# Performance work log

Measured on AMD Instinct MI355X. Metric: run time of the kernel, lower is better.

The kernel has to match this reference:

```python
import jax, jax.numpy as jnp
import numpy as np

N = 100000      # nodes
E = 3_200_000   # edges
F_IN = 256      # input feature dim
R = 16          # rank_bound (GCN output dim)
D = 128         # embedding_dim (trans output)
B = 16384       # batch of node indices
EPS = 1e-5


def setup_inputs() -> dict:
    key = jax.random.key(0)
    ks = jax.random.split(key, 9)
    x = jax.random.normal(ks[0], (N, F_IN), jnp.float32)
    edge_index = jax.random.randint(ks[1], (2, E), 0, N, dtype=jnp.int64)
    trans = jax.random.normal(ks[2], (R, D), jnp.float32) * 0.1
    batch = jax.random.randint(ks[3], (B,), 0, N, dtype=jnp.int64)
    W = jax.random.normal(ks[4], (R, F_IN), jnp.float32) / np.sqrt(F_IN).astype(np.float32)
    b = jnp.zeros((R,), jnp.float32)
    ln_w = jnp.ones((R,), jnp.float32)
    ln_b = jnp.zeros((R,), jnp.float32)
    prelu_a = jnp.full((1,), 0.25, jnp.float32)  # PReLU single shared slope
    return dict(x=x, edge_index=edge_index, trans=trans, batch=batch,
                W=W, b=b, ln_w=ln_w, ln_b=ln_b, prelu_a=prelu_a)


def gcn_conv(x, edge_index, W, b):
    # PyG GCNConv: lin first, then symmetric-normalized aggregation with self-loops.
    h = x @ W.T  # [N, R]
    loop = jnp.arange(N, dtype=edge_index.dtype)
    src = jnp.concatenate([edge_index[0], loop])  # messages flow src -> dst
    dst = jnp.concatenate([edge_index[1], loop])
    deg = jax.ops.segment_sum(jnp.ones_like(dst, h.dtype), dst, num_segments=N)
    dinv = jnp.where(deg > 0, jax.lax.rsqrt(deg), 0.0)
    norm = dinv[src] * dinv[dst]                   # [E+N]
    msg = h[src] * norm[:, None]                   # gather [E+N, R]
    out = jax.ops.segment_sum(msg, dst, num_segments=N)  # scatter-add
    return out + b


def reference(x, edge_index, trans, batch, W, b, ln_w, ln_b, prelu_a):
    h = gcn_conv(x, edge_index, W, b)              # [N, R]
    # PyG LayerNorm (graph mode): normalize over all nodes and channels.
    h = h - h.mean()
    var = (h * h).mean()
    h = h * jax.lax.rsqrt(var + EPS) * ln_w + ln_b
    # PReLU
    h = jnp.where(h >= 0, h, prelu_a * h)
    emb = h @ trans                                # [N, D]
    return emb[batch]                              # index_select(0, batch)
```

## Files before the change

### kernel.cpp

```cpp
#include <hip/hip_runtime.h>

#define EPS 1e-5f
#define BSHIFT 8
#define BSIZE  256
#define NBMAX  512
#define PCHUNK 8192
#define BCAP   16384
#define LCAP   12288

typedef short bf16x8 __attribute__((ext_vector_type(8)));
typedef float f32x4  __attribute__((ext_vector_type(4)));

__device__ __forceinline__ unsigned short f2bf(float f) {
    unsigned u = __float_as_uint(f);
    u += 0x7FFFu + ((u >> 16) & 1u);
    return (unsigned short)(u >> 16);
}
__device__ __forceinline__ float bf2f(unsigned short s) {
    return __uint_as_float(((unsigned)s) << 16);
}
__device__ __forceinline__ void acc8(float* acc, uint4 v) {
    acc[0] += bf2f((unsigned short)(v.x & 0xFFFFu)); acc[1] += bf2f((unsigned short)(v.x >> 16));
    acc[2] += bf2f((unsigned short)(v.y & 0xFFFFu)); acc[3] += bf2f((unsigned short)(v.y >> 16));
    acc[4] += bf2f((unsigned short)(v.z & 0xFFFFu)); acc[5] += bf2f((unsigned short)(v.z >> 16));
    acc[6] += bf2f((unsigned short)(v.w & 0xFFFFu)); acc[7] += bf2f((unsigned short)(v.w >> 16));
}
__device__ __forceinline__ void cvt_hilo(const float* f, bf16x8& hi, bf16x8& lo) {
#pragma unroll
    for (int j = 0; j < 8; j++) {
        unsigned short h = f2bf(f[j]);
        hi[j] = (short)h;
        lo[j] = (short)f2bf(f[j] - bf2f(h));
    }
}

__global__ __launch_bounds__(512) void k_init(unsigned* cursor, int NB) {
    int t = threadIdx.x;
    if (t < NB) cursor[t] = (unsigned)t * BCAP;
}

__global__ __launch_bounds__(512) void k_bpart(const int* __restrict__ ei,
                                               unsigned* __restrict__ cursor,
                                               unsigned* __restrict__ sorted, int E, int NB) {
    __shared__ unsigned cnt[NBMAX];
    __shared__ unsigned lbase[NBMAX];
    __shared__ unsigned loff[NBMAX + 1];
    __shared__ unsigned sh[512];
    __shared__ unsigned stage[PCHUNK];
    __shared__ unsigned short bkt[PCHUNK];
    int t = threadIdx.x;
    for (int i = t; i < NB; i += 512) cnt[i] = 0u;
    __syncthreads();
    const int4* src4 = (const int4*)ei;
    const int4* dst4 = (const int4*)(ei + E);
    int E4 = E >> 2;
    int base4 = blockIdx.x * (PCHUNK / 4);
#pragma unroll
    for (int i = 0; i < PCHUNK / 4 / 512; i++) {
        int idx = base4 + i * 512 + t;
        if (idx < E4) {
            int4 d = dst4[idx];
            atomicAdd(&cnt[d.x >> BSHIFT], 1u);
            atomicAdd(&cnt[d.y >> BSHIFT], 1u);
            atomicAdd(&cnt[d.z >> BSHIFT], 1u);
            atomicAdd(&cnt[d.w >> BSHIFT], 1u);
        }
    }
    __syncthreads();
    unsigned v = (t < NB) ? cnt[t] : 0u;
    sh[t] = v;
    if (t < NB) lbase[t] = v ? atomicAdd(&cursor[t], v) : 0u;
    __syncthreads();
    for (int off = 1; off < 512; off <<= 1) {
        unsigned a = (t >= off) ? sh[t - off] : 0u;
        __syncthreads();
        sh[t] += a;
        __syncthreads();
    }
    if (t < NB) { loff[t] = sh[t] - v; cnt[t] = 0u; }
    if (t == NB - 1) loff[NB] = sh[t];
    __syncthreads();
    for (int b = t; b < NB; b += 512) {
        unsigned s = loff[b], e2 = loff[b + 1];
        for (unsigned j = s; j < e2; j++) bkt[j] = (unsigned short)b;
    }
#pragma unroll
    for (int i = 0; i < PCHUNK / 4 / 512; i++) {
        int idx = base4 + i * 512 + t;
        if (idx < E4) {
            int4 s = src4[idx];
            int4 d = dst4[idx];
            int b; unsigned r;
            b = d.x >> BSHIFT; r = atomicAdd(&cnt[b], 1u);
            stage[loff[b] + r] = (unsigned)s.x | ((unsigned)(d.x & (BSIZE - 1)) << 17);
            b = d.y >> BSHIFT; r = atomicAdd(&cnt[b], 1u);
            stage[loff[b] + r] = (unsigned)s.y | ((unsigned)(d.y & (BSIZE - 1)) << 17);
            b = d.z >> BSHIFT; r = atomicAdd(&cnt[b], 1u);
            stage[loff[b] + r] = (unsigned)s.z | ((unsigned)(d.z & (BSIZE - 1)) << 17);
            b = d.w >> BSHIFT; r = atomicAdd(&cnt[b], 1u);
            stage[loff[b] + r] = (unsigned)s.w | ((unsigned)(d.w & (BSIZE - 1)) << 17);
        }
    }
    __syncthreads();
    unsigned total = loff[NB];
    for (unsigned i = t; i < total; i += 512) {
        unsigned b = bkt[i];
        sorted[lbase[b] + (i - loff[b])] = stage[i];
    }
}

__global__ __launch_bounds__(512) void k_bdeg2(const unsigned* __restrict__ cursor,
                                               const unsigned* __restrict__ sorted,
                                               unsigned* __restrict__ nstart,
                                               float* __restrict__ dinv, int N) {
    __shared__ unsigned deg[BSIZE];
    __shared__ unsigned wsum[4];
    int b = blockIdx.x, t = threadIdx.x;
    if (t < BSIZE) deg[t] = 0u;
    __syncthreads();
    unsigned s0 = (unsigned)b * BCAP, s1 = cursor[b];
    for (unsigned j = s0 + t; j < s1; j += 512)
        atomicAdd(&deg[sorted[j] >> 17], 1u);
    __syncthreads();
    unsigned d0 = 0, inc = 0;
    int lane = t & 63, wid = t >> 6;
    if (t < BSIZE) {
        d0 = deg[t];
        inc = d0;
        for (int off = 1; off < 64; off <<= 1) {
            unsigned u = __shfl_up(inc, off, 64);
            if (lane >= off) inc += u;
        }
        if (lane == 63) wsum[wid] = inc;
    }
    __syncthreads();
    if (t < BSIZE) {
        unsigned wbase = 0;
        for (int w = 0; w < wid; w++) wbase += wsum[w];
        unsigned excl = wbase + inc - d0;
        int node = (b << BSHIFT) + t;
        if (node < N) {
            nstart[node] = s0 + excl;
            dinv[node] = rsqrtf((float)(d0 + 1u));
        }
    }
}

__global__ __launch_bounds__(256, 4) void k_gemm(const float* __restrict__ x,
                                                 const float* __restrict__ W,
                                                 const float* __restrict__ dinv,
                                                 unsigned short* __restrict__ hs,
                                                 int N, int NT) {
    int t = threadIdx.x;
    int w = t >> 6, lane = t & 63;
    int lr = lane & 15;
    int lk = lane >> 4;
    bf16x8 bh[8], bl[8];
#pragma unroll
    for (int kt = 0; kt < 8; kt++) {
        float wf[8];
        const float* wp = W + lr * 256 + kt * 32 + lk * 8;
        *(float4*)&wf[0] = *(const float4*)wp;
        *(float4*)&wf[4] = *(const float4*)(wp + 4);
        cvt_hilo(wf, bh[kt], bl[kt]);
    }
    int nw = gridDim.x * 4;
    int wid = blockIdx.x * 4 + w;
    for (int tile = wid; tile < NT; tile += nw) {
        int nb = tile << 4;
        int node = nb + lr;
        const float* xp = x + (size_t)node * 256;
        f32x4 acc = {0.f, 0.f, 0.f, 0.f};
#pragma unroll
        for (int kt = 0; kt < 8; kt++) {
            float af[8];
            if (node < N) {
                const float* ap = xp + kt * 32 + lk * 8;
                *(float4*)&af[0] = *(const float4*)ap;
                *(float4*)&af[4] = *(const float4*)(ap + 4);
            } else {
#pragma unroll
                for (int j = 0; j < 8; j++) af[j] = 0.f;
            }
            bf16x8 ah, al;
            cvt_hilo(af, ah, al);
            acc = __builtin_amdgcn_mfma_f32_16x16x32_bf16(ah, bh[kt], acc, 0, 0, 0);
            acc = __builtin_amdgcn_mfma_f32_16x16x32_bf16(al, bh[kt], acc, 0, 0, 0);
            acc = __builtin_amdgcn_mfma_f32_16x16x32_bf16(ah, bl[kt], acc, 0, 0, 0);
        }
#pragma unroll
        for (int i = 0; i < 4; i++) {
            int n2 = nb + lk * 4 + i;
            if (n2 < N) {
                float dv = dinv[n2];
                hs[(size_t)n2 * 16 + lr] = f2bf(acc[i] * dv);
            }
        }
    }
}

__global__ __launch_bounds__(512) void k_aggf(const unsigned* __restrict__ cursor,
                                              const unsigned* __restrict__ nstart,
                                              const unsigned* __restrict__ sorted,
                                              const unsigned short* __restrict__ hs,
                                              const float* __restrict__ dinv,
                                              const float* __restrict__ bias,
                                              float* __restrict__ agg,
                                              float2* __restrict__ part,
                                              unsigned* __restrict__ scratch, int N) {
    __shared__ unsigned buf[LCAP];
    __shared__ unsigned cur0[BSIZE + 1];
    __shared__ unsigned curv[BSIZE];
    __shared__ float ss[8], qq[8];
    int b = blockIdx.x, t = threadIdx.x;
    unsigned s0 = (unsigned)b * BCAP, s1 = cursor[b];
    unsigned len = s1 - s0;
    if (t < BSIZE) {
        int node = (b << BSHIFT) + t;
        unsigned ns = (node < N) ? nstart[node] : s1;
        cur0[t] = ns - s0;
        curv[t] = ns - s0;
    }
    if (t == 0) cur0[BSIZE] = len;
    __syncthreads();
    bool fit = (len <= (unsigned)LCAP);
    if (fit) {
        for (unsigned j = t; j < len; j += 512) {
            unsigned u = sorted[s0 + j];
            unsigned pos = atomicAdd(&curv[u >> 17], 1u);
            buf[pos] = u & 0x1FFFFu;
        }
    } else {
        for (unsigned j = t; j < len; j += 512) {
            unsigned u = sorted[s0 + j];
            unsigned pos = atomicAdd(&curv[u >> 17], 1u);
            scratch[s0 + pos] = u & 0x1FFFFu;
        }
    }
    __syncthreads();
    int g = t >> 4, r = t & 15;
    int sub = r >> 1;
    int half = r & 1;
    float sacc = 0.f, qacc = 0.f;
#pragma unroll 1
    for (int p = 0; p < 8; p++) {
        int dloc = p * 32 + g;
        int d = (b << BSHIFT) + dloc;
        float acc[8];
#pragma unroll
        for (int c = 0; c < 8; c++) acc[c] = 0.f;
        if (d < N) {
            unsigned l0 = cur0[dloc], l1 = cur0[dloc + 1];
            for (unsigned j = l0; j < l1; j += 16) {
                unsigned row0 = j + sub, row1 = j + 8 + sub;
                bool p0 = row0 < l1, p1 = row1 < l1;
                unsigned i0 = 0, i1 = 0;
                if (fit) {
                    if (p0) i0 = buf[row0];
                    if (p1) i1 = buf[row1];
                } else {
                    if (p0) i0 = scratch[s0 + row0];
                    if (p1) i1 = scratch[s0 + row1];
                }
                uint4 v0, v1;
                if (p0) v0 = ((const uint4*)(hs + (size_t)i0 * 16))[half];
                if (p1) v1 = ((const uint4*)(hs + (size_t)i1 * 16))[half];
                if (p0) acc8(acc, v0);
                if (p1) acc8(acc, v1);
            }
        }
#pragma unroll
        for (int off = 2; off <= 8; off <<= 1) {
#pragma unroll
            for (int c = 0; c < 8; c++) acc[c] += __shfl_down(acc[c], off, 64);
        }
        if (d < N && r < 2) {
            float dd = dinv[d];
            uint4 hv = ((const uint4*)(hs + (size_t)d * 16))[half];
            float self[8];
            self[0] = bf2f((unsigned short)(hv.x & 0xFFFFu)); self[1] = bf2f((unsigned short)(hv.x >> 16));
            self[2] = bf2f((unsigned short)(hv.y & 0xFFFFu)); self[3] = bf2f((unsigned short)(hv.y >> 16));
            self[4] = bf2f((unsigned short)(hv.z & 0xFFFFu)); self[5] = bf2f((unsigned short)(hv.z >> 16));
            self[6] = bf2f((unsigned short)(hv.w & 0xFFFFu)); self[7] = bf2f((unsigned short)(hv.w >> 16));
            float o[8];
#pragma unroll
            for (int c = 0; c < 8; c++) o[c] = (acc[c] + self[c]) * dd;
            float* an = agg + (size_t)d * 16 + half * 8;
            *(float4*)(an)     = make_float4(o[0], o[1], o[2], o[3]);
            *(float4*)(an + 4) = make_float4(o[4], o[5], o[6], o[7]);
            const float* bp = bias + half * 8;
            float4 b0 = *(const float4*)bp, b1 = *(const float4*)(bp + 4);
            float a0 = o[0] + b0.x, a1 = o[1] + b0.y, a2 = o[2] + b0.z, a3 = o[3] + b0.w;
            float a4 = o[4] + b1.x, a5 = o[5] + b1.y, a6 = o[6] + b1.z, a7 = o[7] + b1.w;
            sacc += (a0 + a1) + (a2 + a3) + (a4 + a5) + (a6 + a7);
            qacc += a0 * a0 + a1 * a1 + a2 * a2 + a3 * a3 + a4 * a4 + a5 * a5 + a6 * a6 + a7 * a7;
        }
    }
    for (int off = 32; off > 0; off >>= 1) {
        sacc += __shfl_down(sacc, off, 64);
        qacc += __shfl_down(qacc, off, 64);
    }
    int lane = t & 63, wid = t >> 6;
    if (lane == 0) { ss[wid] = sacc; qq[wid] = qacc; }
    __syncthreads();
    if (t == 0) {
        float s = 0.f, q = 0.f;
#pragma unroll
        for (int i = 0; i < 8; i++) { s += ss[i]; q += qq[i]; }
        part[b] = make_float2(s, q);
    }
}

__global__ __launch_bounds__(256) void k_final(const float* __restrict__ agg,
                                               const int* __restrict__ batch,
                                               const float* __restrict__ trans,
                                               const float* __restrict__ bias,
                                               const float* __restrict__ ln_w,
                                               const float* __restrict__ ln_b,
                                               const float* __restrict__ prelu_a,
                                               const float2* __restrict__ part,
                                               float* __restrict__ out, int B, float invCnt, int M) {
    __shared__ float tl[16 * 128];
    __shared__ float hh[8 * 16];
    __shared__ float ssr[4], qqr[4];
    const int tid = threadIdx.x;
    for (int i = tid; i < 2048; i += 256) tl[i] = trans[i];
    float s = 0.f, q = 0.f;
    for (int i = tid; i < M; i += 256) {
        float2 v = part[i];
        s += v.x; q += v.y;
    }
    for (int off = 32; off > 0; off >>= 1) {
        s += __shfl_down(s, off, 64);
        q += __shfl_down(q, off, 64);
    }
    int lane = tid & 63, wd = tid >> 6;
    if (lane == 0) { ssr[wd] = s; qqr[wd] = q; }
    __syncthreads();
    float S = ssr[0] + ssr[1] + ssr[2] + ssr[3];
    float Q = qqr[0] + qqr[1] + qqr[2] + qqr[3];
    float mean = S * invCnt;
    float var  = Q * invCnt - mean * mean;
    float inv  = rsqrtf(var + EPS);
    int row0 = blockIdx.x * 8;
    if (tid < 128) {
        int lr = tid >> 4, r = tid & 15;
        int row = row0 + lr;
        if (row < B) {
            int node = batch[row];
            float v = agg[(size_t)node * 16 + r] + bias[r];
            v = (v - mean) * inv * ln_w[r] + ln_b[r];
            float a = prelu_a[0];
            v = v >= 0.f ? v : a * v;
            hh[lr * 16 + r] = v;
        }
    }
    __syncthreads();
    int d = tid & 127, hlf = tid >> 7;
    float tv[16];
#pragma unroll
    for (int r = 0; r < 16; r++) tv[r] = tl[r * 128 + d];
#pragma unroll
    for (int rr = 0; rr < 4; rr++) {
        int lr = rr * 2 + hlf;
        int row = row0 + lr;
        if (row < B) {
            const float* hrow = hh + lr * 16;
            float acc = 0.f;
#pragma unroll
            for (int r = 0; r < 16; r++) acc += hrow[r] * tv[r];
            out[(size_t)row * 128 + d] = acc;
        }
    }
}

extern "C" void kernel_launch(void* const* d_in, const int* in_sizes, int n_in,
                              void* d_out, int out_size, void* d_ws, size_t ws_size,
                              hipStream_t stream) {
    const float* x       = (const float*)d_in[0];
    const int*   ei      = (const int*)d_in[1];
    const float* trans   = (const float*)d_in[2];
    const int*   batch   = (const int*)d_in[3];
    const float* W       = (const float*)d_in[4];
    const float* bias    = (const float*)d_in[5];
    const float* ln_w    = (const float*)d_in[6];
    const float* ln_b    = (const float*)d_in[7];
    const float* prelu_a = (const float*)d_in[8];
    float* out = (float*)d_out;

    const int N = in_sizes[0] / 256;
    const int E = in_sizes[1] / 2;
    const int B = in_sizes[3];
    const int NB = (N + BSIZE - 1) >> BSHIFT;
    const int pbp = (E + PCHUNK - 1) / PCHUNK;
    const int NT = (N + 15) / 16;

    char* p = (char*)d_ws;
    unsigned short* hs = (unsigned short*)p;  p += (size_t)N * 16 * 2;
    float*    agg     = (float*)p;     p += (size_t)N * 16 * 4;
    unsigned* sorted  = (unsigned*)p;  p += (size_t)NB * BCAP * 4;
    unsigned* scratch = (unsigned*)p;  p += (size_t)NB * BCAP * 4;
    float*    dinv    = (float*)p;     p += (size_t)N * 4;
    unsigned* nstart  = (unsigned*)p;  p += (size_t)(N + 1) * 4;
    unsigned* cursor  = (unsigned*)p;  p += NBMAX * 4;
    p = (char*)(((size_t)p + 7) & ~(size_t)7);
    float2*   part    = (float2*)p;    p += (size_t)NB * 8;

    hipLaunchKernelGGL(k_init,  dim3(1),           dim3(512), 0, stream, cursor, NB);
    hipLaunchKernelGGL(k_bpart, dim3(pbp),         dim3(512), 0, stream, ei, cursor, sorted, E, NB);
    hipLaunchKernelGGL(k_bdeg2, dim3(NB),          dim3(512), 0, stream, cursor, sorted, nstart, dinv, N);
    hipLaunchKernelGGL(k_gemm,  dim3(512),         dim3(256), 0, stream, x, W, dinv, hs, N, NT);
    hipLaunchKernelGGL(k_aggf,  dim3(NB),          dim3(512), 0, stream, cursor, nstart, sorted, hs, dinv, bias, agg, part, scratch, N);
    hipLaunchKernelGGL(k_final, dim3((B + 7) / 8), dim3(256), 0, stream, agg, batch, trans, bias,
                       ln_w, ln_b, prelu_a, part, out, B, 1.0f / (float)(N * 16), NB);
}
```

Before: 264.0 us.

## Fold degree computation into partition pass and drop separate degree kernel

Eliminates the k_bdeg2 kernel, which reread the sorted edge buckets to count per-node degrees. Degrees are now counted with global atomics inside the partition kernel. The per-node prefix offsets and inverse sqrt degree are recomputed inside the aggregation kernel, and the GEMM computes rsqrt directly from the degree array. This saves one kernel launch and one pass over the bucketed edges, at the cost of 3.2M global atomic increments on a 100K-entry array and a larger k_init launch to zero it.

Measured after the change: 372.7 us. +41.2%, slower.

```diff
diff --git a/kernel.cpp b/kernel.cpp
--- a/kernel.cpp
+++ b/kernel.cpp
@@ -34,13 +34,16 @@
     }
 }
 
-__global__ __launch_bounds__(512) void k_init(unsigned* cursor, int NB) {
-    int t = threadIdx.x;
-    if (t < NB) cursor[t] = (unsigned)t * BCAP;
+__global__ __launch_bounds__(512) void k_init(unsigned* __restrict__ deg,
+                                              unsigned* __restrict__ cursor, int N, int NB) {
+    int idx = blockIdx.x * 512 + threadIdx.x;
+    if (idx < N) deg[idx] = 0u;
+    if (blockIdx.x == 0 && threadIdx.x < NB) cursor[threadIdx.x] = (unsigned)threadIdx.x * BCAP;
 }
 
 __global__ __launch_bounds__(512) void k_bpart(const int* __restrict__ ei,
                                                unsigned* __restrict__ cursor,
+                                               unsigned* __restrict__ deg,
                                                unsigned* __restrict__ sorted, int E, int NB) {
     __shared__ unsigned cnt[NBMAX];
     __shared__ unsigned lbase[NBMAX];
@@ -64,6 +67,10 @@
             atomicAdd(&cnt[d.y >> BSHIFT], 1u);
             atomicAdd(&cnt[d.z >> BSHIFT], 1u);
             atomicAdd(&cnt[d.w >> BSHIFT], 1u);
+            atomicAdd(&deg[d.x], 1u);
+            atomicAdd(&deg[d.y], 1u);
+            atomicAdd(&deg[d.z], 1u);
+            atomicAdd(&deg[d.w], 1u);
         }
     }
     __syncthreads();
@@ -109,46 +116,9 @@
     }
 }
 
-__global__ __launch_bounds__(512) void k_bdeg2(const unsigned* __restrict__ cursor,
-                                               const unsigned* __restrict__ sorted,
-                                               unsigned* __restrict__ nstart,
-                                               float* __restrict__ dinv, int N) {
-    __shared__ unsigned deg[BSIZE];
-    __shared__ unsigned wsum[4];
-    int b = blockIdx.x, t = threadIdx.x;
-    if (t < BSIZE) deg[t] = 0u;
-    __syncthreads();
-    unsigned s0 = (unsigned)b * BCAP, s1 = cursor[b];
-    for (unsigned j = s0 + t; j < s1; j += 512)
-        atomicAdd(&deg[sorted[j] >> 17], 1u);
-    __syncthreads();
-    unsigned d0 = 0, inc = 0;
-    int lane = t & 63, wid = t >> 6;
-    if (t < BSIZE) {
-        d0 = deg[t];
-        inc = d0;
-        for (int off = 1; off < 64; off <<= 1) {
-            unsigned u = __shfl_up(inc, off, 64);
-            if (lane >= off) inc += u;
-        }
-        if (lane == 63) wsum[wid] = inc;
-    }
-    __syncthreads();
-    if (t < BSIZE) {
-        unsigned wbase = 0;
-        for (int w = 0; w < wid; w++) wbase += wsum[w];
-        unsigned excl = wbase + inc - d0;
-        int node = (b << BSHIFT) + t;
-        if (node < N) {
-            nstart[node] = s0 + excl;
-            dinv[node] = rsqrtf((float)(d0 + 1u));
-        }
-    }
-}
-
 __global__ __launch_bounds__(256, 4) void k_gemm(const float* __restrict__ x,
                                                  const float* __restrict__ W,
-                                                 const float* __restrict__ dinv,
+                                                 const unsigned* __restrict__ deg,
                                                  unsigned short* __restrict__ hs,
                                                  int N, int NT) {
     int t = threadIdx.x;
@@ -192,7 +162,7 @@
         for (int i = 0; i < 4; i++) {
             int n2 = nb + lk * 4 + i;
             if (n2 < N) {
-                float dv = dinv[n2];
+                float dv = rsqrtf((float)(deg[n2] + 1u));
                 hs[(size_t)n2 * 16 + lr] = f2bf(acc[i] * dv);
             }
         }
@@ -200,10 +170,9 @@
 }
 
 __global__ __launch_bounds__(512) void k_aggf(const unsigned* __restrict__ cursor,
-                                              const unsigned* __restrict__ nstart,
+                                              const unsigned* __restrict__ deg,
                                               const unsigned* __restrict__ sorted,
                                               const unsigned short* __restrict__ hs,
-                                              const float* __restrict__ dinv,
                                               const float* __restrict__ bias,
                                               float* __restrict__ agg,
                                               float2* __restrict__ part,
@@ -211,15 +180,32 @@
     __shared__ unsigned buf[LCAP];
     __shared__ unsigned cur0[BSIZE + 1];
     __shared__ unsigned curv[BSIZE];
+    __shared__ float dnv[BSIZE];
+    __shared__ unsigned wsum[4];
     __shared__ float ss[8], qq[8];
     int b = blockIdx.x, t = threadIdx.x;
     unsigned s0 = (unsigned)b * BCAP, s1 = cursor[b];
     unsigned len = s1 - s0;
+    unsigned d0 = 0, inc = 0;
+    int lane = t & 63, wv = t >> 6;
     if (t < BSIZE) {
         int node = (b << BSHIFT) + t;
-        unsigned ns = (node < N) ? nstart[node] : s1;
-        cur0[t] = ns - s0;
-        curv[t] = ns - s0;
+        d0 = (node < N) ? deg[node] : 0u;
+        dnv[t] = rsqrtf((float)(d0 + 1u));
+        inc = d0;
+        for (int off = 1; off < 64; off <<= 1) {
+            unsigned u = __shfl_up(inc, off, 64);
+            if (lane >= off) inc += u;
+        }
+        if (lane == 63) wsum[wv] = inc;
+    }
+    __syncthreads();
+    if (t < BSIZE) {
+        unsigned wbase = 0;
+        for (int w = 0; w < wv; w++) wbase += wsum[w];
+        unsigned excl = wbase + inc - d0;
+        cur0[t] = excl;
+        curv[t] = excl;
     }
     if (t == 0) cur0[BSIZE] = len;
     __syncthreads();
@@ -275,7 +261,7 @@
             for (int c = 0; c < 8; c++) acc[c] += __shfl_down(acc[c], off, 64);
         }
         if (d < N && r < 2) {
-            float dd = dinv[d];
+            float dd = dnv[dloc];
             uint4 hv = ((const uint4*)(hs + (size_t)d * 16))[half];
             float self[8];
             self[0] = bf2f((unsigned short)(hv.x & 0xFFFFu)); self[1] = bf2f((unsigned short)(hv.x >> 16));
@@ -300,8 +286,7 @@
         sacc += __shfl_down(sacc, off, 64);
         qacc += __shfl_down(qacc, off, 64);
     }
-    int lane = t & 63, wid = t >> 6;
-    if (lane == 0) { ss[wid] = sacc; qq[wid] = qacc; }
+    if (lane == 0) { ss[wv] = sacc; qq[wv] = qacc; }
     __syncthreads();
     if (t == 0) {
         float s = 0.f, q = 0.f;
@@ -400,17 +385,15 @@
     float*    agg     = (float*)p;     p += (size_t)N * 16 * 4;
     unsigned* sorted  = (unsigned*)p;  p += (size_t)NB * BCAP * 4;
     unsigned* scratch = (unsigned*)p;  p += (size_t)NB * BCAP * 4;
-    float*    dinv    = (float*)p;     p += (size_t)N * 4;
-    unsigned* nstart  = (unsigned*)p;  p += (size_t)(N + 1) * 4;
+    unsigned* deg     = (unsigned*)p;  p += (size_t)N * 4;
     unsigned* cursor  = (unsigned*)p;  p += NBMAX * 4;
     p = (char*)(((size_t)p + 7) & ~(size_t)7);
     float2*   part    = (float2*)p;    p += (size_t)NB * 8;
 
-    hipLaunchKernelGGL(k_init,  dim3(1),           dim3(512), 0, stream, cursor, NB);
-    hipLaunchKernelGGL(k_bpart, dim3(pbp),         dim3(512), 0, stream, ei, cursor, sorted, E, NB);
-    hipLaunchKernelGGL(k_bdeg2, dim3(NB),          dim3(512), 0, stream, cursor, sorted, nstart, dinv, N);
-    hipLaunchKernelGGL(k_gemm,  dim3(512),         dim3(256), 0, stream, x, W, dinv, hs, N, NT);
-    hipLaunchKernelGGL(k_aggf,  dim3(NB),          dim3(512), 0, stream, cursor, nstart, sorted, hs, dinv, bias, agg, part, scratch, N);
-    hipLaunchKernelGGL(k_final, dim3((B + 7) / 8), dim3(256), 0, stream, agg, batch, trans, bias,
+    hipLaunchKernelGGL(k_init,  dim3((N + 511) / 512), dim3(512), 0, stream, deg, cursor, N, NB);
+    hipLaunchKernelGGL(k_bpart, dim3(pbp),             dim3(512), 0, stream, ei, cursor, deg, sorted, E, NB);
+    hipLaunchKernelGGL(k_gemm,  dim3(512),             dim3(256), 0, stream, x, W, deg, hs, N, NT);
+    hipLaunchKernelGGL(k_aggf,  dim3(NB),              dim3(512), 0, stream, cursor, deg, sorted, hs, bias, agg, part, scratch, N);
+    hipLaunchKernelGGL(k_final, dim3((B + 7) / 8),     dim3(256), 0, stream, agg, batch, trans, bias,
                        ln_w, ln_b, prelu_a, part, out, B, 1.0f / (float)(N * 16), NB);
 }
```
